# Kernel optimization log

Measured on AMD Instinct MI355X. Metric: run time of the kernel, lower is better.

## Reference

```python
import jax, jax.numpy as jnp
import numpy as np

B, N, PREV, PRED, H = 16, 64, 6, 30, 256
E = N * (N - 1)
BN_EPS = 1e-5


def _mlp(x, W1, b1, W2, b2, gamma, beta):
    # Two-layer ELU MLP with batch norm over flattened (batch*rows) dim.
    h = jax.nn.elu(x @ W1 + b1)
    h = jax.nn.elu(h @ W2 + b2)
    b, n, d = h.shape
    f = h.reshape(b * n, d)
    mu = f.mean(axis=0)
    var = f.var(axis=0)
    f = (f - mu) * jax.lax.rsqrt(var + BN_EPS) * gamma + beta
    return f.reshape(b, n, d)


def setup_inputs() -> dict:
    key = jax.random.key(0)
    ks = jax.random.split(key, 8)
    # fully-connected directed graph without self loops
    recv, send = np.where(~np.eye(N, dtype=bool))  # each [E]
    rel_rec = jnp.broadcast_to(jax.nn.one_hot(jnp.asarray(recv), N)[None], (B, E, N)).astype(jnp.float32)
    rel_send = jnp.broadcast_to(jax.nn.one_hot(jnp.asarray(send), N)[None], (B, E, N)).astype(jnp.float32)

    def xavier(k, shape):
        fan_in, fan_out = shape
        std = np.sqrt(2.0 / (fan_in + fan_out))
        return jax.random.normal(k, shape, jnp.float32) * std

    return {
        "prev_actor_centers": jax.random.normal(ks[0], (B, N, PREV, 2), jnp.float32) * 10.0,
        "rel_rec": rel_rec,
        "rel_send": rel_send,
        "W_traj": xavier(ks[1], (PREV * 2, H)),
        "b_traj": jnp.full((H,), 0.1, jnp.float32),
        "n2e_W1": xavier(ks[2], (2 * H, H)),
        "n2e_b1": jnp.full((H,), 0.1, jnp.float32),
        "n2e_W2": xavier(ks[3], (H, H)),
        "n2e_b2": jnp.full((H,), 0.1, jnp.float32),
        "n2e_gamma": jnp.ones((H,), jnp.float32),
        "n2e_beta": jnp.zeros((H,), jnp.float32),
        "e2n_W1": xavier(ks[4], (2 * H, H)),
        "e2n_b1": jnp.full((H,), 0.1, jnp.float32),
        "e2n_W2": xavier(ks[5], (H, H)),
        "e2n_b2": jnp.full((H,), 0.1, jnp.float32),
        "e2n_gamma": jnp.ones((H,), jnp.float32),
        "e2n_beta": jnp.zeros((H,), jnp.float32),
        "W_fuse": xavier(ks[6], (2 * H, H)),
        "b_fuse": jnp.full((H,), 0.1, jnp.float32),
        "W_pred": xavier(ks[7], (H, PRED * 2)),
        "b_pred": jnp.full((PRED * 2,), 0.1, jnp.float32),
    }


def reference(prev_actor_centers, rel_rec, rel_send,
              W_traj, b_traj,
              n2e_W1, n2e_b1, n2e_W2, n2e_b2, n2e_gamma, n2e_beta,
              e2n_W1, e2n_b1, e2n_W2, e2n_b2, e2n_gamma, e2n_beta,
              W_fuse, b_fuse, W_pred, b_pred):
    b, n, prev, _ = prev_actor_centers.shape
    # relative displacements, first step zero
    diffs = prev_actor_centers[:, :, 1:, :] - prev_actor_centers[:, :, :-1, :]
    rel_pos = jnp.concatenate([jnp.zeros((b, n, 1, 2), prev_actor_centers.dtype), diffs], axis=2)
    rel_pos = rel_pos.reshape(b, n, prev * 2)
    x = rel_pos @ W_traj + b_traj  # [b, n, H] node features

    # node2edge: gather via one-hot relation matmuls
    receivers = jnp.einsum('ben,bnh->beh', rel_rec, x)
    senders = jnp.einsum('ben,bnh->beh', rel_send, x)
    edges = jnp.concatenate([receivers, senders], axis=-1)  # [b, E, 2H]
    e = _mlp(edges, n2e_W1, n2e_b1, n2e_W2, n2e_b2, n2e_gamma, n2e_beta)

    # edge2node: degree-normalized scatter via transposed relation matmuls
    deg_rec = rel_rec.sum(axis=1)  # [b, n]
    deg_rec = deg_rec + (deg_rec == 0).astype(deg_rec.dtype)
    incoming = jnp.einsum('ben,beh->bnh', rel_rec, e) / deg_rec[..., None]
    deg_send = rel_send.sum(axis=1)
    deg_send = deg_send + (deg_send == 0).astype(deg_send.dtype)
    outgoing = jnp.einsum('ben,beh->bnh', rel_send, e) / deg_send[..., None]
    nodes = jnp.concatenate([incoming, outgoing], axis=-1)  # [b, n, 2H]
    m = _mlp(nodes, e2n_W1, e2n_b1, e2n_W2, e2n_b2, e2n_gamma, e2n_beta)

    fused = jnp.concatenate([x, m], axis=-1) @ W_fuse + b_fuse  # [b, n, H]
    rel = fused @ W_pred + b_pred  # [b, n, PRED*2]

    current_loc = prev_actor_centers[:, :, -1, :]  # [b, n, 2]
    current_loc = jnp.broadcast_to(current_loc[:, :, None, :], (b, n, PRED, 2)).reshape(b, n, PRED * 2)
    pos = jnp.cumsum(rel.reshape(b, n, PRED, 2), axis=2).reshape(b, n, PRED * 2) + current_loc
    return (rel, pos)
```

## Files before the change

kernel.cpp:

```cpp
#include <hip/hip_runtime.h>
#include <hip/hip_bf16.h>

#define BB 16
#define NN 64
#define PREVN 6
#define PREDN 30
#define HH 256
#define EE 4032
#define EROWS (BB*EE)
#define NROWS (BB*NN)

typedef short short8 __attribute__((ext_vector_type(8)));
typedef float f32x4 __attribute__((ext_vector_type(4)));

enum : int {
  OFF_STATS_E = 0,
  OFF_STATS_M = 1024,
  OFF_XRS     = 2048,
  F32_END     = 264192
};
enum : size_t {
  BO_XB    = 0,
  BO_W1TE  = 262144,
  BO_W2TE  = 393216,
  BO_W1TN  = 458752,
  BO_W2TN  = 589824,
  BO_WFT   = 655360,
  BO_WPT   = 786432,
  BO_NODES = 802816,
  BO_M2    = 1327104,
  BO_E2    = 1589248
};

__device__ __forceinline__ float eluf(float v) { return v > 0.f ? v : expm1f(v); }

__device__ __forceinline__ void gl2lds16(const void* g, void* l) {
  __builtin_amdgcn_global_load_lds(
      (const __attribute__((address_space(1))) void*)g,
      (__attribute__((address_space(3))) void*)l, 16, 0, 0);
}

struct PrepArgs {
  const float *centers, *W_traj, *b_traj;
  const float *n2e_W1, *n2e_W2, *e2n_W1, *e2n_W2, *W_fuse, *W_pred;
  float* stats;
  __hip_bfloat16 *xb, *w1te, *w2te, *w1tn, *w2tn, *wft, *wpt;
};

__global__ __launch_bounds__(256) void k_prep(PrepArgs a) {
  __shared__ float t[64][65];
  const int bid = blockIdx.x, tid = threadIdx.x;
  if (bid < 128) {
    const float* W; __hip_bfloat16* WT; int K, lb;
    if (bid < 32)      { W = a.n2e_W1; WT = a.w1te; K = 512; lb = bid; }
    else if (bid < 48) { W = a.n2e_W2; WT = a.w2te; K = 256; lb = bid - 32; }
    else if (bid < 80) { W = a.e2n_W1; WT = a.w1tn; K = 512; lb = bid - 48; }
    else if (bid < 96) { W = a.e2n_W2; WT = a.w2tn; K = 256; lb = bid - 80; }
    else               { W = a.W_fuse; WT = a.wft;  K = 512; lb = bid - 96; }
    int KB = K / 64;
    int k0 = (lb % KB) * 64, n0 = (lb / KB) * 64;
    int tx = tid & 63, ty = tid >> 6;
    #pragma unroll
    for (int i = 0; i < 16; ++i)
      t[ty + i*4][tx] = W[(size_t)(k0 + ty + i*4) * 256 + n0 + tx];
    __syncthreads();
    #pragma unroll
    for (int i = 0; i < 16; ++i)
      WT[(size_t)(n0 + ty + i*4) * K + k0 + tx] = __float2bfloat16(t[tx][ty + i*4]);
  } else if (bid < 192) {
    int idx = (bid - 128) * 256 + tid;
    int c = idx >> 8, k = idx & 255;
    a.wpt[idx] = __float2bfloat16(c < 60 ? a.W_pred[k * 60 + c] : 0.f);
  } else if (bid < 200) {
    a.stats[(bid - 192) * 256 + tid] = 0.f;
  } else {
    int row = bid - 200, col = tid;
    const float* c = a.centers + row * (PREVN * 2);
    float rp[12];
    #pragma unroll
    for (int t2 = 0; t2 < 5; ++t2) {
      rp[2 + 2*t2] = c[(t2+1)*2 + 0] - c[t2*2 + 0];
      rp[3 + 2*t2] = c[(t2+1)*2 + 1] - c[t2*2 + 1];
    }
    float acc = a.b_traj[col];
    #pragma unroll
    for (int k = 2; k < 12; ++k) acc += rp[k] * a.W_traj[k*HH + col];
    a.xb[row*HH + col] = __float2bfloat16(acc);
  }
}

__global__ __launch_bounds__(256) void k_xrs(
    const __hip_bfloat16* __restrict__ xb,
    const __hip_bfloat16* __restrict__ W1T,
    const float* __restrict__ b1,
    __hip_bfloat16* __restrict__ xrs) {
  const int tid = threadIdx.x;
  const int w = tid >> 6, lane = tid & 63;
  const int m16 = lane & 15, quad = lane >> 4;
  const int ko = quad * 8;
  const int half = blockIdx.x >> 4;
  const int row0 = (blockIdx.x & 15) * 64;
  const int colw = w * 64;
  __hip_bfloat16* dst = xrs + (size_t)half * 262144;

  f32x4 acc[4][4];
  #pragma unroll
  for (int jt = 0; jt < 4; ++jt) {
    float bv = half ? 0.f : b1[colw + jt*16 + m16];
    #pragma unroll
    for (int mt = 0; mt < 4; ++mt) acc[mt][jt] = (f32x4){bv, bv, bv, bv};
  }
  #pragma unroll
  for (int ks = 0; ks < 8; ++ks) {
    short8 af[4], bf[4];
    #pragma unroll
    for (int mt = 0; mt < 4; ++mt)
      af[mt] = *reinterpret_cast<const short8*>(
          xb + (size_t)(row0 + mt*16 + m16)*256 + ks*32 + ko);
    #pragma unroll
    for (int jt = 0; jt < 4; ++jt)
      bf[jt] = *reinterpret_cast<const short8*>(
          W1T + (size_t)(colw + jt*16 + m16)*512 + half*256 + ks*32 + ko);
    #pragma unroll
    for (int mt = 0; mt < 4; ++mt)
      #pragma unroll
      for (int jt = 0; jt < 4; ++jt)
        acc[mt][jt] = __builtin_amdgcn_mfma_f32_16x16x32_bf16(af[mt], bf[jt],
                                                              acc[mt][jt], 0, 0, 0);
  }
  #pragma unroll
  for (int mt = 0; mt < 4; ++mt)
    #pragma unroll
    for (int jt = 0; jt < 4; ++jt)
      #pragma unroll
      for (int r = 0; r < 4; ++r)
        dst[(size_t)(row0 + mt*16 + quad*4 + r)*256 + colw + jt*16 + m16] =
            __float2bfloat16(acc[mt][jt][r]);
}

__global__ __launch_bounds__(256, 2) void k_mlp6(
    const __hip_bfloat16* __restrict__ xrs,
    const __hip_bfloat16* __restrict__ W2T,
    const float* __restrict__ b2,
    __hip_bfloat16* __restrict__ outp,
    float* __restrict__ stats) {
  __shared__ alignas(16) char reg1[33792];
  __shared__ alignas(16) __hip_bfloat16 h1s[64][264];
  const int tid = threadIdx.x;
  const int w = tid >> 6, lane = tid & 63;
  const int m16 = lane & 15, quad = lane >> 4;
  const int ko = quad * 8;
  const int blk = blockIdx.x;
  const int bb = blk / 63, lb = blk - bb*63;
  const int row0 = blk * 64;
  const int n0 = (lb * 64) / 63;
  const int colw = w * 64;
  const int csub = lane >> 3, jl = lane & 7;
  const int jsrc = jl ^ csub;
  const int swz0 = ((quad)     ^ (m16 & 7)) * 16;
  const int swz1 = ((quad + 4) ^ (m16 & 7)) * 16;

  const char* xsb = (const char*)(xrs + 262144 + (size_t)bb*64*256);
  #pragma unroll
  for (int i = 0; i < 8; ++i) {
    int seg = w*8 + i;
    gl2lds16(xsb + seg*1024 + lane*16, reg1 + seg*1024);
  }
  if (w == 0)
    gl2lds16((const char*)(xrs + (size_t)(bb*64 + n0)*256) + lane*16, reg1 + 32768);
  __syncthreads();

  {
    const int ty = tid >> 7;
    const int c2 = (tid & 127) * 2;
    #pragma unroll 4
    for (int r2 = 0; r2 < 32; ++r2) {
      int r = ty*32 + r2;
      int e = lb*64 + r;
      int rc = e / 63; int jj = e - rc*63;
      int sd = jj + (jj >= rc ? 1 : 0);
      __hip_bfloat162 xa = *reinterpret_cast<const __hip_bfloat162*>(
          reg1 + 32768 + (rc - n0)*512 + c2*2);
      __hip_bfloat162 xs2 = *reinterpret_cast<const __hip_bfloat162*>(
          reg1 + sd*512 + c2*2);
      __hip_bfloat162 o;
      o.x = __float2bfloat16(eluf(__bfloat162float(xa.x) + __bfloat162float(xs2.x)));
      o.y = __float2bfloat16(eluf(__bfloat162float(xa.y) + __bfloat162float(xs2.y)));
      *reinterpret_cast<__hip_bfloat162*>(&h1s[r][c2]) = o;
    }
  }
  __syncthreads();

  __hip_bfloat16* Wt = (__hip_bfloat16*)reg1;
  f32x4 acc2[4][4];
  #pragma unroll
  for (int jt = 0; jt < 4; ++jt) {
    float bv = b2[colw + jt*16 + m16];
    #pragma unroll
    for (int mt = 0; mt < 4; ++mt) acc2[mt][jt] = (f32x4){bv, bv, bv, bv};
  }
  for (int kt = 0; kt < 4; ++kt) {
    const int k0 = kt * 64;
    #pragma unroll
    for (int i = 0; i < 8; ++i) {
      const __hip_bfloat16* gp = W2T + (size_t)(colw + i*8 + csub) * 256 + k0 + jsrc*8;
      gl2lds16(gp, (char*)Wt + w*8192 + i*1024);
    }
    __syncthreads();
    #pragma unroll
    for (int ks = 0; ks < 2; ++ks) {
      const int sw = ks ? swz1 : swz0;
      short8 af[4], bf[4];
      #pragma unroll
      for (int mt = 0; mt < 4; ++mt)
        af[mt] = *(const short8*)((const char*)h1s +
                     (size_t)(mt*16 + m16)*528 + (k0 + ks*32 + ko)*2);
      #pragma unroll
      for (int jt = 0; jt < 4; ++jt)
        bf[jt] = *(const short8*)((const char*)Wt + (colw + jt*16 + m16)*128 + sw);
      #pragma unroll
      for (int mt = 0; mt < 4; ++mt)
        #pragma unroll
        for (int jt = 0; jt < 4; ++jt)
          acc2[mt][jt] = __builtin_amdgcn_mfma_f32_16x16x32_bf16(af[mt], bf[jt],
                                                                 acc2[mt][jt], 0, 0, 0);
    }
    __syncthreads();
  }
  #pragma unroll
  for (int mt = 0; mt < 4; ++mt)
    #pragma unroll
    for (int jt = 0; jt < 4; ++jt)
      #pragma unroll
      for (int r = 0; r < 4; ++r)
        h1s[mt*16 + quad*4 + r][colw + jt*16 + m16] =
            __float2bfloat16(eluf(acc2[mt][jt][r]));
  __syncthreads();

  {
    float s = 0.f, q = 0.f;
    #pragma unroll 8
    for (int r = 0; r < 64; ++r) {
      float v = __bfloat162float(h1s[r][tid]);
      s += v; q += v * v;
    }
    atomicAdd(&stats[tid], s);
    atomicAdd(&stats[256 + tid], q);
  }
  #pragma unroll
  for (int i = 0; i < 8; ++i) {
    int u = i*256 + tid;
    int r = u >> 5, c = (u & 31) * 8;
    *reinterpret_cast<uint4*>(outp + (size_t)(row0 + r)*HH + c) =
        *reinterpret_cast<const uint4*>(&h1s[r][c]);
  }
}

__global__ __launch_bounds__(256, 2) void k_mlp3n(
    const __hip_bfloat16* __restrict__ A,
    const __hip_bfloat16* __restrict__ W1T,
    const float* __restrict__ b1,
    const __hip_bfloat16* __restrict__ W2T,
    const float* __restrict__ b2,
    __hip_bfloat16* __restrict__ outp,
    float* __restrict__ stats) {
  __shared__ alignas(16) __hip_bfloat16 Wt[256 * 64];
  __shared__ alignas(16) __hip_bfloat16 At[16 * 64];
  __shared__ alignas(16) __hip_bfloat16 h1s[16][264];
  const int tid = threadIdx.x;
  const int w = tid >> 6, lane = tid & 63;
  const int m16 = lane & 15, quad = lane >> 4;
  const int ko = quad * 8;
  const int row0 = blockIdx.x * 16;
  const int colw = w * 64;
  const int csub = lane >> 3, jl = lane & 7;
  const int jsrc = jl ^ csub;
  const int swz0 = ((quad)     ^ (m16 & 7)) * 16;
  const int swz1 = ((quad + 4) ^ (m16 & 7)) * 16;

  const __hip_bfloat16 *ar0 = nullptr, *ar1 = nullptr;
  if (w < 2) {
    int r = w * 8 + csub;
    ar0 = A + (size_t)(row0 + r) * 512;
    ar1 = ar0 + 256;
  }

  f32x4 acc[4];
  #pragma unroll
  for (int jt = 0; jt < 4; ++jt) {
    float bv = b1[colw + jt*16 + m16];
    acc[jt] = (f32x4){bv, bv, bv, bv};
  }
  for (int kt = 0; kt < 8; ++kt) {
    const int k0 = kt * 64;
    #pragma unroll
    for (int i = 0; i < 8; ++i) {
      const __hip_bfloat16* gp = W1T + (size_t)(colw + i*8 + csub) * 512 + k0 + jsrc*8;
      gl2lds16(gp, (char*)Wt + w*8192 + i*1024);
    }
    if (w < 2) {
      const __hip_bfloat16* gp = (k0 < 256 ? ar0 + k0 : ar1 + (k0 - 256)) + jsrc*8;
      gl2lds16(gp, (char*)At + w*1024);
    }
    __syncthreads();
    #pragma unroll
    for (int ks = 0; ks < 2; ++ks) {
      const int sw = ks ? swz1 : swz0;
      short8 af = *(const short8*)((const char*)At + m16*128 + sw);
      short8 bf[4];
      #pragma unroll
      for (int jt = 0; jt < 4; ++jt)
        bf[jt] = *(const short8*)((const char*)Wt + (colw + jt*16 + m16)*128 + sw);
      #pragma unroll
      for (int jt = 0; jt < 4; ++jt)
        acc[jt] = __builtin_amdgcn_mfma_f32_16x16x32_bf16(af, bf[jt], acc[jt], 0, 0, 0);
    }
    __syncthreads();
  }
  #pragma unroll
  for (int jt = 0; jt < 4; ++jt)
    #pragma unroll
    for (int r = 0; r < 4; ++r)
      h1s[quad*4 + r][colw + jt*16 + m16] = __float2bfloat16(eluf(acc[jt][r]));
  __syncthreads();

  f32x4 acc2[4];
  #pragma unroll
  for (int jt = 0; jt < 4; ++jt) {
    float bv = b2[colw + jt*16 + m16];
    acc2[jt] = (f32x4){bv, bv, bv, bv};
  }
  for (int kt = 0; kt < 4; ++kt) {
    const int k0 = kt * 64;
    #pragma unroll
    for (int i = 0; i < 8; ++i) {
      const __hip_bfloat16* gp = W2T + (size_t)(colw + i*8 + csub) * 256 + k0 + jsrc*8;
      gl2lds16(gp, (char*)Wt + w*8192 + i*1024);
    }
    __syncthreads();
    #pragma unroll
    for (int ks = 0; ks < 2; ++ks) {
      const int sw = ks ? swz1 : swz0;
      short8 af = *(const short8*)((const char*)h1s +
                     (size_t)m16*528 + (k0 + ks*32 + ko)*2);
      short8 bf[4];
      #pragma unroll
      for (int jt = 0; jt < 4; ++jt)
        bf[jt] = *(const short8*)((const char*)Wt + (colw + jt*16 + m16)*128 + sw);
      #pragma unroll
      for (int jt = 0; jt < 4; ++jt)
        acc2[jt] = __builtin_amdgcn_mfma_f32_16x16x32_bf16(af, bf[jt], acc2[jt], 0, 0, 0);
    }
    __syncthreads();
  }
  #pragma unroll
  for (int jt = 0; jt < 4; ++jt)
    #pragma unroll
    for (int r = 0; r < 4; ++r)
      h1s[quad*4 + r][colw + jt*16 + m16] = __float2bfloat16(eluf(acc2[jt][r]));
  __syncthreads();

  {
    float s = 0.f, q = 0.f;
    #pragma unroll 8
    for (int r = 0; r < 16; ++r) {
      float v = __bfloat162float(h1s[r][tid]);
      s += v; q += v * v;
    }
    atomicAdd(&stats[tid], s);
    atomicAdd(&stats[256 + tid], q);
  }
  #pragma unroll
  for (int i = 0; i < 2; ++i) {
    int u = i*256 + tid;
    int r = u >> 5, c = (u & 31) * 8;
    *reinterpret_cast<uint4*>(outp + (size_t)(row0 + r)*HH + c) =
        *reinterpret_cast<const uint4*>(&h1s[r][c]);
  }
}

__global__ __launch_bounds__(256) void k_agg2(const __hip_bfloat16* __restrict__ e2,
                                              const float* __restrict__ st,
                                              const float* __restrict__ gam,
                                              const float* __restrict__ bet,
                                              __hip_bfloat16* __restrict__ nodes) {
  __shared__ float red[8][256];
  const int blk = blockIdx.x;
  const int bn = blk >> 1, half = blk & 1;
  const int b = bn >> 6, n = bn & 63;
  const int tid = threadIdx.x;
  const int c8 = (tid & 31) * 8;
  const int rg = tid >> 5;
  const __hip_bfloat16* base = e2 + (size_t)b * EE * HH;
  float s[8] = {0.f,0.f,0.f,0.f,0.f,0.f,0.f,0.f};
  for (int j = rg; j < 63; j += 8) {
    const __hip_bfloat16* rp;
    if (half == 0) {
      rp = base + (size_t)(n*63 + j)*HH;
    } else {
      int i = j + (j >= n ? 1 : 0);
      int e = i*63 + n - (n > i ? 1 : 0);
      rp = base + (size_t)e*HH;
    }
    union { uint4 u; __hip_bfloat16 h[8]; } v;
    v.u = *reinterpret_cast<const uint4*>(rp + c8);
    #pragma unroll
    for (int jj = 0; jj < 8; ++jj) s[jj] += __bfloat162float(v.h[jj]);
  }
  #pragma unroll
  for (int jj = 0; jj < 8; jj += 4)
    *reinterpret_cast<float4*>(&red[rg][c8 + jj]) =
        (float4){s[jj], s[jj+1], s[jj+2], s[jj+3]};
  __syncthreads();
  float S = 0.f;
  #pragma unroll
  for (int r = 0; r < 8; ++r) S += red[r][tid];
  const float inv = 1.f / (float)EROWS;
  float mean = st[tid] * inv;
  float var  = fmaxf(st[256 + tid] * inv - mean*mean, 0.f);
  float a = gam[tid] * rsqrtf(var + 1e-5f);
  float c0 = bet[tid] - mean * a;
  nodes[(size_t)bn*512 + half*256 + tid] = __float2bfloat16(a * S * (1.f/63.f) + c0);
}

__global__ __launch_bounds__(256) void k_head2(
    const __hip_bfloat16* __restrict__ xb,
    const __hip_bfloat16* __restrict__ m2,
    const float* __restrict__ stM,
    const float* __restrict__ gam,
    const float* __restrict__ bet,
    const __hip_bfloat16* __restrict__ WfT,
    const float* __restrict__ bfv,
    const __hip_bfloat16* __restrict__ WpT,
    const float* __restrict__ bp,
    const float* __restrict__ centers,
    float* __restrict__ out) {
  __shared__ alignas(16) __hip_bfloat16 hs[16][264];
  __shared__ float rl[16][64];
  __shared__ float bnA[256], bnC[256];
  const int tid = threadIdx.x;
  const int w = tid >> 6, lane = tid & 63;
  const int m16 = lane & 15, quad = lane >> 4;
  const int ko = quad * 8;
  const int row0 = blockIdx.x * 16;
  const int colw = w * 64;

  {
    const float inv = 1.f / (float)NROWS;
    float mean = stM[tid] * inv;
    float var  = fmaxf(stM[256 + tid] * inv - mean*mean, 0.f);
    float am = gam[tid] * rsqrtf(var + 1e-5f);
    bnA[tid] = am;
    bnC[tid] = bet[tid] - mean * am;
  }
  __syncthreads();

  f32x4 acc[4];
  #pragma unroll
  for (int jt = 0; jt < 4; ++jt) {
    float bv = bfv[colw + jt*16 + m16];
    acc[jt] = (f32x4){bv, bv, bv, bv};
  }
  #pragma unroll
  for (int ks = 0; ks < 16; ++ks) {
    short8 af;
    if (ks < 8) {
      af = *reinterpret_cast<const short8*>(
          xb + (size_t)(row0 + m16)*256 + ks*32 + ko);
    } else {
      int k0 = (ks - 8)*32 + ko;
      union { uint4 u; __hip_bfloat16 h[8]; } v;
      v.u = *reinterpret_cast<const uint4*>(m2 + (size_t)(row0 + m16)*256 + k0);
      union { short8 s8; __hip_bfloat16 h[8]; } o;
      #pragma unroll
      for (int j = 0; j < 8; ++j)
        o.h[j] = __float2bfloat16(bnA[k0+j] * __bfloat162float(v.h[j]) + bnC[k0+j]);
      af = o.s8;
    }
    short8 bf[4];
    #pragma unroll
    for (int jt = 0; jt < 4; ++jt)
      bf[jt] = *reinterpret_cast<const short8*>(
          WfT + (size_t)(colw + jt*16 + m16)*512 + ks*32 + ko);
    #pragma unroll
    for (int jt = 0; jt < 4; ++jt)
      acc[jt] = __builtin_amdgcn_mfma_f32_16x16x32_bf16(af, bf[jt], acc[jt], 0, 0, 0);
  }
  #pragma unroll
  for (int jt = 0; jt < 4; ++jt)
    #pragma unroll
    for (int r = 0; r < 4; ++r)
      hs[quad*4 + r][colw + jt*16 + m16] = __float2bfloat16(acc[jt][r]);
  __syncthreads();

  if (w == 0) {
    f32x4 acc2[4];
    #pragma unroll
    for (int jt = 0; jt < 4; ++jt) {
      int c = jt*16 + m16;
      float bv = (c < 60) ? bp[c] : 0.f;
      acc2[jt] = (f32x4){bv, bv, bv, bv};
    }
    #pragma unroll
    for (int ks = 0; ks < 8; ++ks) {
      short8 af = *reinterpret_cast<const short8*>(&hs[m16][ks*32 + ko]);
      short8 bf[4];
      #pragma unroll
      for (int jt = 0; jt < 4; ++jt)
        bf[jt] = *reinterpret_cast<const short8*>(
            WpT + (size_t)(jt*16 + m16)*256 + ks*32 + ko);
      #pragma unroll
      for (int jt = 0; jt < 4; ++jt)
        acc2[jt] = __builtin_amdgcn_mfma_f32_16x16x32_bf16(af, bf[jt], acc2[jt], 0, 0, 0);
    }
    #pragma unroll
    for (int jt = 0; jt < 4; ++jt) {
      int c = jt*16 + m16;
      #pragma unroll
      for (int r = 0; r < 4; ++r) {
        int lr = quad*4 + r;
        rl[lr][c] = acc2[jt][r];
        if (c < 60) out[(size_t)(row0 + lr)*60 + c] = acc2[jt][r];
      }
    }
  }
  __syncthreads();

  if (tid < 32) {
    int lr = tid >> 1, xy = tid & 1;
    int grow = row0 + lr;
    float run = centers[(size_t)(grow*PREVN + 5)*2 + xy];
    #pragma unroll
    for (int p = 0; p < PREDN; ++p) {
      run += rl[lr][2*p + xy];
      out[61440 + (size_t)grow*60 + 2*p + xy] = run;
    }
  }
}

extern "C" void kernel_launch(void* const* d_in, const int* in_sizes, int n_in,
                              void* d_out, int out_size, void* d_ws, size_t ws_size,
                              hipStream_t stream) {
  const float* centers = (const float*)d_in[0];
  float* ws = (float*)d_ws;
  __hip_bfloat16* wb = (__hip_bfloat16*)(ws + F32_END);
  __hip_bfloat16* xrs = (__hip_bfloat16*)(ws + OFF_XRS);

  PrepArgs pa;
  pa.centers = centers;
  pa.W_traj = (const float*)d_in[3];  pa.b_traj = (const float*)d_in[4];
  pa.n2e_W1 = (const float*)d_in[5];  pa.n2e_W2 = (const float*)d_in[7];
  pa.e2n_W1 = (const float*)d_in[11]; pa.e2n_W2 = (const float*)d_in[13];
  pa.W_fuse = (const float*)d_in[17]; pa.W_pred = (const float*)d_in[19];
  pa.stats = ws;
  pa.xb = wb + BO_XB; pa.w1te = wb + BO_W1TE; pa.w2te = wb + BO_W2TE;
  pa.w1tn = wb + BO_W1TN; pa.w2tn = wb + BO_W2TN; pa.wft = wb + BO_WFT;
  pa.wpt = wb + BO_WPT;

  const float* n2e_b1 = (const float*)d_in[6];
  const float* n2e_b2 = (const float*)d_in[8];
  const float* n2e_g  = (const float*)d_in[9];
  const float* n2e_be = (const float*)d_in[10];
  const float* e2n_b1 = (const float*)d_in[12];
  const float* e2n_b2 = (const float*)d_in[14];
  const float* e2n_g  = (const float*)d_in[15];
  const float* e2n_be = (const float*)d_in[16];
  const float* b_fuse = (const float*)d_in[18];
  const float* b_pred = (const float*)d_in[20];

  k_prep<<<1224, 256, 0, stream>>>(pa);
  k_xrs<<<32, 256, 0, stream>>>(wb + BO_XB, wb + BO_W1TE, n2e_b1, xrs);
  k_mlp6<<<EROWS/64, 256, 0, stream>>>(xrs, wb + BO_W2TE, n2e_b2,
                                       wb + BO_E2, ws + OFF_STATS_E);
  k_agg2<<<2*NROWS, 256, 0, stream>>>(wb + BO_E2, ws + OFF_STATS_E, n2e_g, n2e_be,
                                      wb + BO_NODES);
  k_mlp3n<<<NROWS/16, 256, 0, stream>>>(wb + BO_NODES, wb + BO_W1TN, e2n_b1,
                                        wb + BO_W2TN, e2n_b2,
                                        wb + BO_M2, ws + OFF_STATS_M);
  k_head2<<<NROWS/16, 256, 0, stream>>>(wb + BO_XB, wb + BO_M2, ws + OFF_STATS_M,
                                        e2n_g, e2n_be, wb + BO_WFT, b_fuse,
                                        wb + BO_WPT, b_pred, centers,
                                        (float*)d_out);
}
```

Baseline: 210.7 us.

## Fuse trajectory embedding into consumers, read W2 directly, widen aggregation blocks

The trajectory embedding is now recomputed inside k_xrs and k_head2 and kept in LDS, so the bf16 xb buffer and its prep blocks disappear. The W2 staging through LDS (global_load_lds plus barriers per k-tile) in the edge and node MLP kernels is replaced by direct global short8 loads, removing the per-tile syncs. The aggregation kernel grows to 1024 threads so each block handles the 63 edge rows with more parallel row groups. The trade-off is redundant embedding compute and more L2 traffic for W2 reads in the hot edge MLP.

```diff
diff --git a/kernel.cpp b/kernel.cpp
--- a/kernel.cpp
+++ b/kernel.cpp
@@ -20,7 +20,6 @@
   F32_END     = 264192
 };
 enum : size_t {
-  BO_XB    = 0,
   BO_W1TE  = 262144,
   BO_W2TE  = 393216,
   BO_W1TN  = 458752,
@@ -40,11 +39,25 @@
       (__attribute__((address_space(3))) void*)l, 16, 0, 0);
 }
 
+__device__ __forceinline__ float xembed(const float* __restrict__ centers,
+                                        const float* __restrict__ Wt,
+                                        const float* __restrict__ bt,
+                                        int rr, int col) {
+  const float* c = centers + rr * 12;
+  float acc = bt[col];
+  #pragma unroll
+  for (int t = 0; t < 5; ++t) {
+    float dx = c[(t+1)*2 + 0] - c[t*2 + 0];
+    float dy = c[(t+1)*2 + 1] - c[t*2 + 1];
+    acc += dx * Wt[(2 + 2*t)*HH + col] + dy * Wt[(3 + 2*t)*HH + col];
+  }
+  return acc;
+}
+
 struct PrepArgs {
-  const float *centers, *W_traj, *b_traj;
   const float *n2e_W1, *n2e_W2, *e2n_W1, *e2n_W2, *W_fuse, *W_pred;
   float* stats;
-  __hip_bfloat16 *xb, *w1te, *w2te, *w1tn, *w2tn, *wft, *wpt;
+  __hip_bfloat16 *w1te, *w2te, *w1tn, *w2tn, *wft, *wpt;
 };
 
 __global__ __launch_bounds__(256) void k_prep(PrepArgs a) {
@@ -71,29 +84,19 @@
     int idx = (bid - 128) * 256 + tid;
     int c = idx >> 8, k = idx & 255;
     a.wpt[idx] = __float2bfloat16(c < 60 ? a.W_pred[k * 60 + c] : 0.f);
-  } else if (bid < 200) {
+  } else {
     a.stats[(bid - 192) * 256 + tid] = 0.f;
-  } else {
-    int row = bid - 200, col = tid;
-    const float* c = a.centers + row * (PREVN * 2);
-    float rp[12];
-    #pragma unroll
-    for (int t2 = 0; t2 < 5; ++t2) {
-      rp[2 + 2*t2] = c[(t2+1)*2 + 0] - c[t2*2 + 0];
-      rp[3 + 2*t2] = c[(t2+1)*2 + 1] - c[t2*2 + 1];
-    }
-    float acc = a.b_traj[col];
-    #pragma unroll
-    for (int k = 2; k < 12; ++k) acc += rp[k] * a.W_traj[k*HH + col];
-    a.xb[row*HH + col] = __float2bfloat16(acc);
   }
 }
 
 __global__ __launch_bounds__(256) void k_xrs(
-    const __hip_bfloat16* __restrict__ xb,
+    const float* __restrict__ centers,
+    const float* __restrict__ W_traj,
+    const float* __restrict__ b_traj,
     const __hip_bfloat16* __restrict__ W1T,
     const float* __restrict__ b1,
     __hip_bfloat16* __restrict__ xrs) {
+  __shared__ alignas(16) __hip_bfloat16 xls[64][264];
   const int tid = threadIdx.x;
   const int w = tid >> 6, lane = tid & 63;
   const int m16 = lane & 15, quad = lane >> 4;
@@ -103,6 +106,10 @@
   const int colw = w * 64;
   __hip_bfloat16* dst = xrs + (size_t)half * 262144;
 
+  for (int r = 0; r < 64; ++r)
+    xls[r][tid] = __float2bfloat16(xembed(centers, W_traj, b_traj, row0 + r, tid));
+  __syncthreads();
+
   f32x4 acc[4][4];
   #pragma unroll
   for (int jt = 0; jt < 4; ++jt) {
@@ -115,8 +122,7 @@
     short8 af[4], bf[4];
     #pragma unroll
     for (int mt = 0; mt < 4; ++mt)
-      af[mt] = *reinterpret_cast<const short8*>(
-          xb + (size_t)(row0 + mt*16 + m16)*256 + ks*32 + ko);
+      af[mt] = *reinterpret_cast<const short8*>(&xls[mt*16 + m16][ks*32 + ko]);
     #pragma unroll
     for (int jt = 0; jt < 4; ++jt)
       bf[jt] = *reinterpret_cast<const short8*>(
@@ -155,10 +161,6 @@
   const int row0 = blk * 64;
   const int n0 = (lb * 64) / 63;
   const int colw = w * 64;
-  const int csub = lane >> 3, jl = lane & 7;
-  const int jsrc = jl ^ csub;
-  const int swz0 = ((quad)     ^ (m16 & 7)) * 16;
-  const int swz1 = ((quad + 4) ^ (m16 & 7)) * 16;
 
   const char* xsb = (const char*)(xrs + 262144 + (size_t)bb*64*256);
   #pragma unroll
@@ -191,7 +193,6 @@
   }
   __syncthreads();
 
-  __hip_bfloat16* Wt = (__hip_bfloat16*)reg1;
   f32x4 acc2[4][4];
   #pragma unroll
   for (int jt = 0; jt < 4; ++jt) {
@@ -199,25 +200,20 @@
     #pragma unroll
     for (int mt = 0; mt < 4; ++mt) acc2[mt][jt] = (f32x4){bv, bv, bv, bv};
   }
+  #pragma unroll
   for (int kt = 0; kt < 4; ++kt) {
-    const int k0 = kt * 64;
-    #pragma unroll
-    for (int i = 0; i < 8; ++i) {
-      const __hip_bfloat16* gp = W2T + (size_t)(colw + i*8 + csub) * 256 + k0 + jsrc*8;
-      gl2lds16(gp, (char*)Wt + w*8192 + i*1024);
-    }
-    __syncthreads();
     #pragma unroll
     for (int ks = 0; ks < 2; ++ks) {
-      const int sw = ks ? swz1 : swz0;
+      const int k0 = kt*64 + ks*32 + ko;
       short8 af[4], bf[4];
+      #pragma unroll
+      for (int jt = 0; jt < 4; ++jt)
+        bf[jt] = *reinterpret_cast<const short8*>(
+            W2T + (size_t)(colw + jt*16 + m16)*256 + k0);
       #pragma unroll
       for (int mt = 0; mt < 4; ++mt)
         af[mt] = *(const short8*)((const char*)h1s +
-                     (size_t)(mt*16 + m16)*528 + (k0 + ks*32 + ko)*2);
-      #pragma unroll
-      for (int jt = 0; jt < 4; ++jt)
-        bf[jt] = *(const short8*)((const char*)Wt + (colw + jt*16 + m16)*128 + sw);
+                     (size_t)(mt*16 + m16)*528 + k0*2);
       #pragma unroll
       for (int mt = 0; mt < 4; ++mt)
         #pragma unroll
@@ -225,8 +221,8 @@
           acc2[mt][jt] = __builtin_amdgcn_mfma_f32_16x16x32_bf16(af[mt], bf[jt],
                                                                  acc2[mt][jt], 0, 0, 0);
     }
-    __syncthreads();
-  }
+  }
+  __syncthreads();
   #pragma unroll
   for (int mt = 0; mt < 4; ++mt)
     #pragma unroll
@@ -330,29 +326,23 @@
     float bv = b2[colw + jt*16 + m16];
     acc2[jt] = (f32x4){bv, bv, bv, bv};
   }
+  #pragma unroll
   for (int kt = 0; kt < 4; ++kt) {
-    const int k0 = kt * 64;
-    #pragma unroll
-    for (int i = 0; i < 8; ++i) {
-      const __hip_bfloat16* gp = W2T + (size_t)(colw + i*8 + csub) * 256 + k0 + jsrc*8;
-      gl2lds16(gp, (char*)Wt + w*8192 + i*1024);
-    }
-    __syncthreads();
     #pragma unroll
     for (int ks = 0; ks < 2; ++ks) {
-      const int sw = ks ? swz1 : swz0;
-      short8 af = *(const short8*)((const char*)h1s +
-                     (size_t)m16*528 + (k0 + ks*32 + ko)*2);
+      const int k0 = kt*64 + ks*32 + ko;
+      short8 af = *(const short8*)((const char*)h1s + (size_t)m16*528 + k0*2);
       short8 bf[4];
       #pragma unroll
       for (int jt = 0; jt < 4; ++jt)
-        bf[jt] = *(const short8*)((const char*)Wt + (colw + jt*16 + m16)*128 + sw);
+        bf[jt] = *reinterpret_cast<const short8*>(
+            W2T + (size_t)(colw + jt*16 + m16)*256 + k0);
       #pragma unroll
       for (int jt = 0; jt < 4; ++jt)
         acc2[jt] = __builtin_amdgcn_mfma_f32_16x16x32_bf16(af, bf[jt], acc2[jt], 0, 0, 0);
     }
-    __syncthreads();
-  }
+  }
+  __syncthreads();
   #pragma unroll
   for (int jt = 0; jt < 4; ++jt)
     #pragma unroll
@@ -379,12 +369,12 @@
   }
 }
 
-__global__ __launch_bounds__(256) void k_agg2(const __hip_bfloat16* __restrict__ e2,
-                                              const float* __restrict__ st,
-                                              const float* __restrict__ gam,
-                                              const float* __restrict__ bet,
-                                              __hip_bfloat16* __restrict__ nodes) {
-  __shared__ float red[8][256];
+__global__ __launch_bounds__(1024) void k_agg2(const __hip_bfloat16* __restrict__ e2,
+                                               const float* __restrict__ st,
+                                               const float* __restrict__ gam,
+                                               const float* __restrict__ bet,
+                                               __hip_bfloat16* __restrict__ nodes) {
+  __shared__ float red[32][256];
   const int blk = blockIdx.x;
   const int bn = blk >> 1, half = blk & 1;
   const int b = bn >> 6, n = bn & 63;
@@ -393,7 +383,7 @@
   const int rg = tid >> 5;
   const __hip_bfloat16* base = e2 + (size_t)b * EE * HH;
   float s[8] = {0.f,0.f,0.f,0.f,0.f,0.f,0.f,0.f};
-  for (int j = rg; j < 63; j += 8) {
+  for (int j = rg; j < 63; j += 32) {
     const __hip_bfloat16* rp;
     if (half == 0) {
       rp = base + (size_t)(n*63 + j)*HH;
@@ -412,19 +402,23 @@
     *reinterpret_cast<float4*>(&red[rg][c8 + jj]) =
         (float4){s[jj], s[jj+1], s[jj+2], s[jj+3]};
   __syncthreads();
-  float S = 0.f;
-  #pragma unroll
-  for (int r = 0; r < 8; ++r) S += red[r][tid];
-  const float inv = 1.f / (float)EROWS;
-  float mean = st[tid] * inv;
-  float var  = fmaxf(st[256 + tid] * inv - mean*mean, 0.f);
-  float a = gam[tid] * rsqrtf(var + 1e-5f);
-  float c0 = bet[tid] - mean * a;
-  nodes[(size_t)bn*512 + half*256 + tid] = __float2bfloat16(a * S * (1.f/63.f) + c0);
+  if (tid < 256) {
+    float S = 0.f;
+    #pragma unroll
+    for (int r = 0; r < 32; ++r) S += red[r][tid];
+    const float inv = 1.f / (float)EROWS;
+    float mean = st[tid] * inv;
+    float var  = fmaxf(st[256 + tid] * inv - mean*mean, 0.f);
+    float a = gam[tid] * rsqrtf(var + 1e-5f);
+    float c0 = bet[tid] - mean * a;
+    nodes[(size_t)bn*512 + half*256 + tid] = __float2bfloat16(a * S * (1.f/63.f) + c0);
+  }
 }
 
 __global__ __launch_bounds__(256) void k_head2(
-    const __hip_bfloat16* __restrict__ xb,
+    const float* __restrict__ centers,
+    const float* __restrict__ W_traj,
+    const float* __restrict__ b_traj,
     const __hip_bfloat16* __restrict__ m2,
     const float* __restrict__ stM,
     const float* __restrict__ gam,
@@ -433,8 +427,8 @@
     const float* __restrict__ bfv,
     const __hip_bfloat16* __restrict__ WpT,
     const float* __restrict__ bp,
-    const float* __restrict__ centers,
     float* __restrict__ out) {
+  __shared__ alignas(16) __hip_bfloat16 xs[16][264];
   __shared__ alignas(16) __hip_bfloat16 hs[16][264];
   __shared__ float rl[16][64];
   __shared__ float bnA[256], bnC[256];
@@ -453,6 +447,9 @@
     bnA[tid] = am;
     bnC[tid] = bet[tid] - mean * am;
   }
+  #pragma unroll
+  for (int r = 0; r < 16; ++r)
+    xs[r][tid] = __float2bfloat16(xembed(centers, W_traj, b_traj, row0 + r, tid));
   __syncthreads();
 
   f32x4 acc[4];
@@ -465,8 +462,7 @@
   for (int ks = 0; ks < 16; ++ks) {
     short8 af;
     if (ks < 8) {
-      af = *reinterpret_cast<const short8*>(
-          xb + (size_t)(row0 + m16)*256 + ks*32 + ko);
+      af = *reinterpret_cast<const short8*>(&xs[m16][ks*32 + ko]);
     } else {
       int k0 = (ks - 8)*32 + ko;
       union { uint4 u; __hip_bfloat16 h[8]; } v;
@@ -546,17 +542,8 @@
   __hip_bfloat16* wb = (__hip_bfloat16*)(ws + F32_END);
   __hip_bfloat16* xrs = (__hip_bfloat16*)(ws + OFF_XRS);
 
-  PrepArgs pa;
-  pa.centers = centers;
-  pa.W_traj = (const float*)d_in[3];  pa.b_traj = (const float*)d_in[4];
-  pa.n2e_W1 = (const float*)d_in[5];  pa.n2e_W2 = (const float*)d_in[7];
-  pa.e2n_W1 = (const float*)d_in[11]; pa.e2n_W2 = (const float*)d_in[13];
-  pa.W_fuse = (const float*)d_in[17]; pa.W_pred = (const float*)d_in[19];
-  pa.stats = ws;
-  pa.xb = wb + BO_XB; pa.w1te = wb + BO_W1TE; pa.w2te = wb + BO_W2TE;
-  pa.w1tn = wb + BO_W1TN; pa.w2tn = wb + BO_W2TN; pa.wft = wb + BO_WFT;
-  pa.wpt = wb + BO_WPT;
-
+  const float* W_traj = (const float*)d_in[3];
+  const float* b_traj = (const float*)d_in[4];
   const float* n2e_b1 = (const float*)d_in[6];
   const float* n2e_b2 = (const float*)d_in[8];
   const float* n2e_g  = (const float*)d_in[9];
@@ -568,17 +555,26 @@
   const float* b_fuse = (const float*)d_in[18];
   const float* b_pred = (const float*)d_in[20];
 
-  k_prep<<<1224, 256, 0, stream>>>(pa);
-  k_xrs<<<32, 256, 0, stream>>>(wb + BO_XB, wb + BO_W1TE, n2e_b1, xrs);
+  PrepArgs pa;
+  pa.n2e_W1 = (const float*)d_in[5];  pa.n2e_W2 = (const float*)d_in[7];
+  pa.e2n_W1 = (const float*)d_in[11]; pa.e2n_W2 = (const float*)d_in[13];
+  pa.W_fuse = (const float*)d_in[17]; pa.W_pred = (const float*)d_in[19];
+  pa.stats = ws;
+  pa.w1te = wb + BO_W1TE; pa.w2te = wb + BO_W2TE;
+  pa.w1tn = wb + BO_W1TN; pa.w2tn = wb + BO_W2TN;
+  pa.wft = wb + BO_WFT;   pa.wpt = wb + BO_WPT;
+
+  k_prep<<<200, 256, 0, stream>>>(pa);
+  k_xrs<<<32, 256, 0, stream>>>(centers, W_traj, b_traj, wb + BO_W1TE, n2e_b1, xrs);
   k_mlp6<<<EROWS/64, 256, 0, stream>>>(xrs, wb + BO_W2TE, n2e_b2,
                                        wb + BO_E2, ws + OFF_STATS_E);
-  k_agg2<<<2*NROWS, 256, 0, stream>>>(wb + BO_E2, ws + OFF_STATS_E, n2e_g, n2e_be,
-                                      wb + BO_NODES);
+  k_agg2<<<2*NROWS, 1024, 0, stream>>>(wb + BO_E2, ws + OFF_STATS_E, n2e_g, n2e_be,
+                                       wb + BO_NODES);
   k_mlp3n<<<NROWS/16, 256, 0, stream>>>(wb + BO_NODES, wb + BO_W1TN, e2n_b1,
                                         wb + BO_W2TN, e2n_b2,
                                         wb + BO_M2, ws + OFF_STATS_M);
-  k_head2<<<NROWS/16, 256, 0, stream>>>(wb + BO_XB, wb + BO_M2, ws + OFF_STATS_M,
-                                        e2n_g, e2n_be, wb + BO_WFT, b_fuse,
-                                        wb + BO_WPT, b_pred, centers,
+  k_head2<<<NROWS/16, 256, 0, stream>>>(centers, W_traj, b_traj, wb + BO_M2,
+                                        ws + OFF_STATS_M, e2n_g, e2n_be,
+                                        wb + BO_WFT, b_fuse, wb + BO_WPT, b_pred,
                                         (float*)d_out);
 }
```

After: 224.2 us. 6.4% more time.
